# Optimization experiments

Hardware: AMD Instinct MI355X
Metric: run time of the kernel (lower is better)

The kernel has to match this reference:

```python
import jax, jax.numpy as jnp
import numpy as np

B, N, E, F_IN, F_OUT, HEADS, HDIM = 64, 1024, 16384, 300, 8, 4, 32
ALPHA = 0.5
BETA = float(np.log(0.1 / 2 + 1.0))  # GCN2Conv: theta=0.1, layer=2


def _norm(src, dst, ew, n):
    # GCN normalization with added self loops: D^-1/2 (A + I) D^-1/2, edge-list form
    idx = jnp.arange(n)
    r = jnp.concatenate([src, idx])
    c = jnp.concatenate([dst, idx])
    w = jnp.concatenate([ew, jnp.ones((n,), ew.dtype)])
    deg = jax.ops.segment_sum(w, c, num_segments=n)  # deg >= 1 (self loop weight 1)
    dinv = jax.lax.rsqrt(jnp.maximum(deg, 1e-12))
    return r, c, dinv[r] * w * dinv[c]


def _prop(h, r, c, w, n):
    # out[c] += w * h[r]  (source-to-target message passing)
    return jax.ops.segment_sum(w[:, None] * h[r], c, num_segments=n)


def _forward(edge_index, x, edge_weight, W1, b1, W2, b2, W3, b3, W4, b4, Wl, Wr, att, bg, Wg1, Wm, bm, Wg2, Wp1, bp1, Wp2, bp2, Wo, bo):
    def per_graph(xg, ei, ewg):
        src, dst = ei[0], ei[1]
        n = xg.shape[0]
        r, c, w = _norm(src, dst, ewg, n)                    # weighted gcn norm
        r1, c1, w1 = _norm(src, dst, jnp.ones_like(ewg), n)  # unweighted gcn norm
        h1 = jax.nn.relu(_prop(xg @ W1, r, c, w, n) + b1)    # [n,256]
        h2 = jax.nn.relu(_prop(h1 @ W2, r, c, w, n) + b2)    # [n,128]
        h = jax.nn.relu(_prop(h2 @ W3, r, c, w, n) + b3)     # [n,64]
        h = jax.nn.relu(_prop(h @ W4, r, c, w, n) + b4)      # [n,32]
        # GATv2Conv(32, 32, heads=4), self loops, concat heads, eval mode (no dropout)
        idx = jnp.arange(n)
        s2, d2 = jnp.concatenate([src, idx]), jnp.concatenate([dst, idx])
        xl = (h @ Wl).reshape(n, HEADS, HDIM)  # source transform
        xr = (h @ Wr).reshape(n, HEADS, HDIM)  # target transform
        e = jax.nn.leaky_relu(xl[s2] + xr[d2], 0.2)          # [E2,H,C]
        lg = jnp.einsum('ehc,hc->eh', e, att)                # [E2,H]
        mx = jax.ops.segment_max(lg, d2, num_segments=n)
        a = jnp.exp(lg - mx[d2])
        alpha = a / jax.ops.segment_sum(a, d2, num_segments=n)[d2]
        h = jax.ops.segment_sum(alpha[..., None] * xl[s2], d2, num_segments=n).reshape(n, HEADS * HDIM) + bg
        h = jax.nn.relu(h)                                   # [n,128]
        # GCN2Conv(128, alpha=0.5, theta=0.1, layer=2), x0 = h2, shared weights, no bias
        z = (1.0 - ALPHA) * _prop(h, r, c, w, n) + ALPHA * h2
        h = jax.nn.relu((1.0 - BETA) * z + BETA * (z @ Wg1))
        # GCNConv(128, 256) called WITHOUT edge weights
        h = jax.nn.relu(_prop(h @ Wm, r1, c1, w1, n) + bm)
        # GCN2Conv(256, 0.5, 0.1, 2), x0 = h1
        z = (1.0 - ALPHA) * _prop(h, r, c, w, n) + ALPHA * h1
        h = jax.nn.relu((1.0 - BETA) * z + BETA * (z @ Wg2))  # [n,256]
        # dense_diff_pool stage 1: GCNConv(256,5) soft assignments + to_dense_adj
        s = jax.nn.softmax(_prop(h @ Wp1, r, c, w, n) + bp1, axis=-1)  # [n,5]
        adj = jnp.zeros((n, n), h.dtype).at[src, dst].add(ewg)
        nodes = s.T @ h                                      # [5,256]
        adj2 = s.T @ adj @ s                                 # [5,5]
        # DenseGCNConv(256,1): set diag to 1, sym-normalize, propagate
        di = jnp.arange(5)
        adjl = adj2.at[di, di].set(1.0)
        dd = jax.lax.rsqrt(jnp.maximum(adjl.sum(-1), 1.0))
        sc = jax.nn.softmax((dd[:, None] * adjl * dd[None, :]) @ (nodes @ Wp2) + bp2, axis=-1)  # [5,1]
        # dense_diff_pool stage 2
        return (sc.T @ nodes)[0]                             # [256]

    pooled = jax.vmap(per_graph)(x, edge_index, edge_weight)  # [B,256]
    return pooled @ Wo + bo


def setup_inputs():
    key = jax.random.key(0)
    ks = jax.random.split(key, 32)
    lin = lambda k, fi, fo: jax.random.normal(k, (fi, fo), jnp.float32) / np.sqrt(fi)
    return {
        'x': jax.random.normal(ks[0], (B, N, F_IN), jnp.float32),
        'edge_index': jax.random.randint(ks[1], (B, 2, E), 0, N),
        'edge_weight': jax.random.uniform(ks[2], (B, E), jnp.float32),
        'W1': lin(ks[3], F_IN, 256), 'b1': jnp.zeros((256,), jnp.float32),
        'W2': lin(ks[4], 256, 128), 'b2': jnp.zeros((128,), jnp.float32),
        'W3': lin(ks[5], 128, 64), 'b3': jnp.zeros((64,), jnp.float32),
        'W4': lin(ks[6], 64, 32), 'b4': jnp.zeros((32,), jnp.float32),
        'Wl': lin(ks[7], 32, 128), 'Wr': lin(ks[8], 32, 128),
        'att': jax.random.normal(ks[9], (HEADS, HDIM), jnp.float32) / np.sqrt(HDIM),
        'bg': jnp.zeros((128,), jnp.float32),
        'Wg1': lin(ks[10], 128, 128),
        'Wm': lin(ks[11], 128, 256), 'bm': jnp.zeros((256,), jnp.float32),
        'Wg2': lin(ks[12], 256, 256),
        'Wp1': lin(ks[13], 256, 5), 'bp1': jnp.zeros((5,), jnp.float32),
        'Wp2': lin(ks[14], 256, 1), 'bp2': jnp.zeros((1,), jnp.float32),
        'Wo': lin(ks[15], 256, F_OUT), 'bo': jnp.zeros((F_OUT,), jnp.float32),
    }


def reference(x, edge_index, edge_weight, W1, b1, W2, b2, W3, b3, W4, b4, Wl, Wr, att, bg, Wg1, Wm, bm, Wg2, Wp1, bp1, Wp2, bp2, Wo, bo):
    return _forward(edge_index, x, edge_weight, W1, b1, W2, b2, W3, b3, W4, b4, Wl, Wr, att, bg, Wg1, Wm, bm, Wg2, Wp1, bp1, Wp2, bp2, Wo, bo)
```

## Files before the change

kernel.cpp:

```cpp
#include <hip/hip_runtime.h>
#include <cstdint>
#include <cstddef>

constexpr int NB = 64;
constexpr int NN = 1024;
constexpr int NE = 16384;
constexpr int NCH = 8;
constexpr int CHE = NE / NCH;
constexpr float C_BETA = 0.04879016417f;

typedef __attribute__((ext_vector_type(8))) short s8v;
typedef __attribute__((ext_vector_type(4))) float f4v;

__device__ inline float bf2f(ushort u){ union{uint u;float f;} v; v.u=((uint)u)<<16; return v.f; }
__device__ inline ushort f2bf(float f){ union{float f;uint u;} v; v.f=f; uint r=v.u+0x7fffu+((v.u>>16)&1u); return (ushort)(r>>16); }
__device__ inline void up8(uint4 x, float* o){
  o[0]=bf2f((ushort)x.x); o[1]=bf2f((ushort)(x.x>>16));
  o[2]=bf2f((ushort)x.y); o[3]=bf2f((ushort)(x.y>>16));
  o[4]=bf2f((ushort)x.z); o[5]=bf2f((ushort)(x.z>>16));
  o[6]=bf2f((ushort)x.w); o[7]=bf2f((ushort)(x.w>>16));
}
__device__ inline uint pk2(float a, float b){ return (uint)f2bf(a) | ((uint)f2bf(b)<<16); }
__device__ inline uint4 pk8(const float* f){
  uint4 v; v.x=pk2(f[0],f[1]); v.y=pk2(f[2],f[3]); v.z=pk2(f[4],f[5]); v.w=pk2(f[6],f[7]); return v;
}
__device__ inline int swz8(int bid, int bpg){
  int xcd = bid & 7, j = bid >> 3;
  return (xcd * (NB/8) + j / bpg) * bpg + (j % bpg);
}


__global__ __launch_bounds__(256) void hist_k(const int* __restrict__ ei,
    const float* __restrict__ ew, int* __restrict__ phist, float* __restrict__ pdegw) {
  int blk = blockIdx.x;
  int b = blk >> 3, ch = blk & 7;
  __shared__ int hc[NN];
  __shared__ float hw[NN];
  int t = threadIdx.x;
  for (int i = t; i < NN; i += 256) { hc[i] = 0; hw[i] = 0.f; }
  __syncthreads();
  const int* dstb = ei + (size_t)b * 2 * NE + NE + ch * CHE;
  const float* ewb = ew + (size_t)b * NE + ch * CHE;
  for (int e = t; e < CHE; e += 256) {
    int d = dstb[e];
    atomicAdd(&hc[d], 1);
    atomicAdd(&hw[d], ewb[e]);
  }
  __syncthreads();
  size_t o = ((size_t)b * NCH + ch) * NN;
  for (int i = t; i < NN; i += 256) {
    phist[o + i] = hc[i];
    pdegw[o + i] = hw[i];
  }
}


__global__ __launch_bounds__(1024) void scan2_k(int* __restrict__ phist,
    const float* __restrict__ pdegw, float* __restrict__ dinvw,
    float* __restrict__ dinvu, int* __restrict__ rowptr) {
  int b = blockIdx.x, t = threadIdx.x;
  size_t base = (size_t)b * NCH * NN;
  int h[NCH];
  int cnt = 0; float dw = 1.0f;
#pragma unroll
  for (int c = 0; c < NCH; ++c) {
    h[c] = phist[base + c * NN + t];
    cnt += h[c];
    dw += pdegw[base + c * NN + t];
  }
  dinvw[b * NN + t] = rsqrtf(dw);
  dinvu[b * NN + t] = rsqrtf(1.0f + (float)cnt);
  __shared__ int ss[NN];
  ss[t] = cnt;
  __syncthreads();
  for (int off = 1; off < NN; off <<= 1) {
    int xv = (t >= off) ? ss[t - off] : 0;
    __syncthreads();
    ss[t] += xv;
    __syncthreads();
  }
  rowptr[b * (NN + 1) + t + 1] = ss[t];
  if (t == 0) rowptr[b * (NN + 1)] = 0;
  int excl = ss[t] - cnt;
#pragma unroll
  for (int c = 0; c < NCH; ++c) {
    phist[base + c * NN + t] = excl;
    excl += h[c];
  }
}


__global__ __launch_bounds__(256) void scatter2_k(const int* __restrict__ ei,
    const float* __restrict__ ew, const int* __restrict__ coff,
    const float* __restrict__ dinvw, const float* __restrict__ dinvu,
    int4* __restrict__ pedge) {
  int blk = blockIdx.x;
  int b = blk >> 3, ch = blk & 7;
  __shared__ int sbase[NN];
  __shared__ int sfill[NN];
  __shared__ float sdw[NN];
  __shared__ float sdu[NN];
  int t = threadIdx.x;
  for (int i = t; i < NN; i += 256) {
    sbase[i] = coff[((size_t)b * NCH + ch) * NN + i];
    sfill[i] = 0;
    sdw[i] = dinvw[b * NN + i];
    sdu[i] = dinvu[b * NN + i];
  }
  __syncthreads();
  const int* srcb = ei + (size_t)b * 2 * NE + ch * CHE;
  const int* dstb = ei + (size_t)b * 2 * NE + NE + ch * CHE;
  const float* ewb = ew + (size_t)b * NE + ch * CHE;
  int4* peb = pedge + (size_t)b * NE;
  for (int e = t; e < CHE; e += 256) {
    int s = srcb[e], d = dstb[e];
    int pos = sbase[d] + atomicAdd(&sfill[d], 1);
    int4 pk;
    pk.x = s;
    pk.y = __float_as_int(sdw[s] * ewb[e] * sdw[d]);
    pk.z = __float_as_int(sdu[s] * sdu[d]);
    pk.w = 0;
    peb[pos] = pk;
  }
}


__global__ void xconv_k(const float* __restrict__ x, ushort* __restrict__ xbf) {
  int g = blockIdx.x * 256 + threadIdx.x;
  int row = g / 40, c = (g % 40) * 8;
  float f[8];
  const float* xr = x + (size_t)row * 300;
  if (c + 8 <= 300) {
    float4 a = *(const float4*)&xr[c];
    float4 bq = *(const float4*)&xr[c + 4];
    f[0]=a.x; f[1]=a.y; f[2]=a.z; f[3]=a.w;
    f[4]=bq.x; f[5]=bq.y; f[6]=bq.z; f[7]=bq.w;
  } else {
#pragma unroll
    for (int j = 0; j < 8; ++j) f[j] = (c + j < 300) ? xr[c + j] : 0.f;
  }
  *(uint4*)&xbf[(size_t)row * 320 + c] = pk8(f);
}

__device__ inline void wcv(const float* __restrict__ W, ushort* __restrict__ Wt,
                           int idx, int K, int N, int Kp) {
  int n = idx / Kp, k = idx % Kp;
  Wt[idx] = (k < K) ? f2bf(W[(size_t)k * N + n]) : (ushort)0;
}

__global__ void wconv_all_k(const float* W1, const float* W2, const float* W3,
                            const float* W4, const float* Wl, const float* Wr,
                            const float* Wg1, const float* Wm, const float* Wg2,
                            ushort* Wt1, ushort* Wt2, ushort* Wt3, ushort* Wt4,
                            ushort* WtLR, ushort* Wtg1, ushort* Wtm, ushort* Wtg2) {
  int bb = blockIdx.x, t = threadIdx.x;
  if      (bb < 320) wcv(W1, Wt1, bb * 256 + t, 300, 256, 320);
  else if (bb < 448) wcv(W2, Wt2, (bb - 320) * 256 + t, 256, 128, 256);
  else if (bb < 480) wcv(W3, Wt3, (bb - 448) * 256 + t, 128, 64, 128);
  else if (bb < 488) wcv(W4, Wt4, (bb - 480) * 256 + t, 64, 32, 64);
  else if (bb < 504) wcv(Wl, WtLR, (bb - 488) * 256 + t, 32, 128, 32);
  else if (bb < 520) wcv(Wr, WtLR + 128 * 32, (bb - 504) * 256 + t, 32, 128, 32);
  else if (bb < 584) wcv(Wg1, Wtg1, (bb - 520) * 256 + t, 128, 128, 128);
  else if (bb < 712) wcv(Wm, Wtm, (bb - 584) * 256 + t, 128, 256, 128);
  else               wcv(Wg2, Wtg2, (bb - 712) * 256 + t, 256, 256, 256);
}


template<int NI, int MODE>
__global__ __launch_bounds__(256) void mgemm_k(const ushort* __restrict__ A,
    const ushort* __restrict__ Bt, const ushort* __restrict__ Z,
    ushort* __restrict__ C, int M, int K, int N) {
  constexpr int BN = NI * 32;
  __shared__ ushort As[128][40];
  __shared__ ushort Bs[BN][40];
  int tid = threadIdx.x;
  int wave = tid >> 6, lane = tid & 63;
  int bm = blockIdx.y * 128, bn = blockIdx.x * BN;
  int wm = (wave >> 1) * 64, wn = (wave & 1) * (NI * 16);
  f4v acc[4][NI];
#pragma unroll
  for (int a = 0; a < 4; ++a)
#pragma unroll
    for (int b = 0; b < NI; ++b)
#pragma unroll
      for (int q = 0; q < 4; ++q) acc[a][b][q] = 0.f;
  int r = lane & 15, kg = (lane >> 4) * 8;
  for (int k0 = 0; k0 < K; k0 += 32) {
#pragma unroll
    for (int c = tid; c < 512; c += 256) {
      int row = c >> 2, kc = (c & 3) * 8;
      *(uint4*)&As[row][kc] = *(const uint4*)&A[(size_t)(bm + row) * K + k0 + kc];
    }
#pragma unroll
    for (int c = tid; c < BN * 4; c += 256) {
      int col = c >> 2, kc = (c & 3) * 8;
      *(uint4*)&Bs[col][kc] = *(const uint4*)&Bt[(size_t)(bn + col) * K + k0 + kc];
    }
    __syncthreads();
    s8v af[4], bf[NI];
#pragma unroll
    for (int mi = 0; mi < 4; ++mi) af[mi] = *(const s8v*)&As[wm + mi * 16 + r][kg];
#pragma unroll
    for (int ni = 0; ni < NI; ++ni) bf[ni] = *(const s8v*)&Bs[wn + ni * 16 + r][kg];
#pragma unroll
    for (int mi = 0; mi < 4; ++mi)
#pragma unroll
      for (int ni = 0; ni < NI; ++ni)
        acc[mi][ni] = __builtin_amdgcn_mfma_f32_16x16x32_bf16(af[mi], bf[ni], acc[mi][ni], 0, 0, 0);
    __syncthreads();
  }
  int col = lane & 15, rowg = (lane >> 4) * 4;
#pragma unroll
  for (int mi = 0; mi < 4; ++mi)
#pragma unroll
    for (int ni = 0; ni < NI; ++ni)
#pragma unroll
      for (int q = 0; q < 4; ++q) {
        int row = bm + wm + mi * 16 + rowg + q;
        int cc = bn + wn + ni * 16 + col;
        size_t idx = (size_t)row * N + cc;
        float v = acc[mi][ni][q];
        if (MODE == 2) v = fmaxf((1.f - C_BETA) * bf2f(Z[idx]) + C_BETA * v, 0.f);
        C[idx] = f2bf(v);
      }
}


template<int D, int MODE, int WSEL>
__global__ __launch_bounds__(256) void prop_k(const ushort* __restrict__ in,
    ushort* __restrict__ out, const int4* __restrict__ pedge,
    const float* __restrict__ dinv, const int* __restrict__ rowptr,
    const float* __restrict__ bias, const ushort* __restrict__ x0) {
  constexpr int TPN = D / 8, NPB = 256 / TPN, BPG = NN / NPB;
  int t = threadIdx.x;
  int bid = swz8(blockIdx.x, BPG);
  int tn = t / TPN, cl = t % TPN;
  int node = bid * NPB + tn;
  int b = node >> 10, i = node & 1023;
  float di = dinv[node];
  float f[8], acc[8];
  uint4 ov = *(const uint4*)&in[(size_t)node * D + cl * 8];
  up8(ov, f);
  float w0 = di * di;
#pragma unroll
  for (int j = 0; j < 8; ++j) acc[j] = w0 * f[j];
  int r0 = rowptr[b * (NN + 1) + i], r1 = rowptr[b * (NN + 1) + i + 1];
  const int4* pe = pedge + (size_t)b * NE;
  const ushort* inb = in + (size_t)b * NN * D;
  int p = r0;
  for (; p + 4 <= r1; p += 4) {
    int4 e0 = pe[p], e1 = pe[p + 1], e2 = pe[p + 2], e3 = pe[p + 3];
    float wa = __int_as_float(WSEL ? e0.z : e0.y);
    float wb2 = __int_as_float(WSEL ? e1.z : e1.y);
    float wc = __int_as_float(WSEL ? e2.z : e2.y);
    float wd = __int_as_float(WSEL ? e3.z : e3.y);
    uint4 rv0 = *(const uint4*)&inb[(size_t)e0.x * D + cl * 8];
    uint4 rv1 = *(const uint4*)&inb[(size_t)e1.x * D + cl * 8];
    uint4 rv2 = *(const uint4*)&inb[(size_t)e2.x * D + cl * 8];
    uint4 rv3 = *(const uint4*)&inb[(size_t)e3.x * D + cl * 8];
    up8(rv0, f);
#pragma unroll
    for (int j = 0; j < 8; ++j) acc[j] += wa * f[j];
    up8(rv1, f);
#pragma unroll
    for (int j = 0; j < 8; ++j) acc[j] += wb2 * f[j];
    up8(rv2, f);
#pragma unroll
    for (int j = 0; j < 8; ++j) acc[j] += wc * f[j];
    up8(rv3, f);
#pragma unroll
    for (int j = 0; j < 8; ++j) acc[j] += wd * f[j];
  }
  for (; p < r1; ++p) {
    int4 e = pe[p];
    float w = __int_as_float(WSEL ? e.z : e.y);
    uint4 rv = *(const uint4*)&inb[(size_t)e.x * D + cl * 8];
    up8(rv, f);
#pragma unroll
    for (int j = 0; j < 8; ++j) acc[j] += w * f[j];
  }
  size_t ob = (size_t)node * D + cl * 8;
  if (MODE == 0) {
#pragma unroll
    for (int j = 0; j < 8; ++j) acc[j] = fmaxf(acc[j] + bias[cl * 8 + j], 0.f);
  } else {
    uint4 xv = *(const uint4*)&x0[ob];
    up8(xv, f);
#pragma unroll
    for (int j = 0; j < 8; ++j) acc[j] = 0.5f * acc[j] + 0.5f * f[j];
  }
  *(uint4*)&out[ob] = pk8(acc);
}


__global__ __launch_bounds__(256) void gat_fused_k(const ushort* __restrict__ xlr,
    const int4* __restrict__ pedge, const int* __restrict__ rowptr,
    const float* __restrict__ att, const float* __restrict__ bg,
    ushort* __restrict__ out) {
  int bid = swz8(blockIdx.x, NN / 16);
  int t = threadIdx.x;
  int tn = t >> 4, cl = t & 15;
  int node = bid * 16 + tn;
  int b = node >> 10, i = node & 1023;
  int ch = cl * 8;
  int r0 = rowptr[b * (NN + 1) + i], r1 = rowptr[b * (NN + 1) + i + 1];
  const ushort* xb = xlr + (size_t)b * NN * 256;
  const int4* pe = pedge + (size_t)b * NE;
  float fr[8], at[8];
  {
    uint4 rv = *(const uint4*)&xb[(size_t)i * 256 + 128 + ch];
    up8(rv, fr);
#pragma unroll
    for (int j = 0; j < 8; ++j) at[j] = att[ch + j];
  }
  float m, den, acc[8];
  {
    float fs[8];
    uint4 sv = *(const uint4*)&xb[(size_t)i * 256 + ch];
    up8(sv, fs);
    float part = 0.f;
#pragma unroll
    for (int j = 0; j < 8; ++j) {
      float v = fs[j] + fr[j];
      v = v > 0.f ? v : 0.2f * v;
      part += v * at[j];
    }
    part += __shfl_xor(part, 1);
    part += __shfl_xor(part, 2);
    m = part; den = 1.f;
#pragma unroll
    for (int j = 0; j < 8; ++j) acc[j] = fs[j];
  }
  float fl0[8], fl1[8];
  int p = r0;
  for (; p + 2 <= r1; p += 2) {
    int s0 = pe[p].x, s1 = pe[p + 1].x;
    uint4 v0 = *(const uint4*)&xb[(size_t)s0 * 256 + ch];
    uint4 v1 = *(const uint4*)&xb[(size_t)s1 * 256 + ch];
    up8(v0, fl0); up8(v1, fl1);
    float p0 = 0.f, p1 = 0.f;
#pragma unroll
    for (int j = 0; j < 8; ++j) {
      float a0 = fl0[j] + fr[j]; a0 = a0 > 0.f ? a0 : 0.2f * a0;
      float a1 = fl1[j] + fr[j]; a1 = a1 > 0.f ? a1 : 0.2f * a1;
      p0 += a0 * at[j]; p1 += a1 * at[j];
    }
    p0 += __shfl_xor(p0, 1); p0 += __shfl_xor(p0, 2);
    p1 += __shfl_xor(p1, 1); p1 += __shfl_xor(p1, 2);
    {
      float mn = fmaxf(m, p0);
      float sc = __expf(m - mn), ex = __expf(p0 - mn);
      den = den * sc + ex;
#pragma unroll
      for (int j = 0; j < 8; ++j) acc[j] = acc[j] * sc + ex * fl0[j];
      m = mn;
    }
    {
      float mn = fmaxf(m, p1);
      float sc = __expf(m - mn), ex = __expf(p1 - mn);
      den = den * sc + ex;
#pragma unroll
      for (int j = 0; j < 8; ++j) acc[j] = acc[j] * sc + ex * fl1[j];
      m = mn;
    }
  }
  if (p < r1) {
    int s = pe[p].x;
    uint4 v0 = *(const uint4*)&xb[(size_t)s * 256 + ch];
    up8(v0, fl0);
    float p0 = 0.f;
#pragma unroll
    for (int j = 0; j < 8; ++j) {
      float a0 = fl0[j] + fr[j]; a0 = a0 > 0.f ? a0 : 0.2f * a0;
      p0 += a0 * at[j];
    }
    p0 += __shfl_xor(p0, 1); p0 += __shfl_xor(p0, 2);
    float mn = fmaxf(m, p0);
    float sc = __expf(m - mn), ex = __expf(p0 - mn);
    den = den * sc + ex;
#pragma unroll
    for (int j = 0; j < 8; ++j) acc[j] = acc[j] * sc + ex * fl0[j];
    m = mn;
  }
  float inv = 1.f / den;
#pragma unroll
  for (int j = 0; j < 8; ++j) acc[j] = fmaxf(acc[j] * inv + bg[ch + j], 0.f);
  *(uint4*)&out[(size_t)node * 128 + ch] = pk8(acc);
}


__global__ __launch_bounds__(256) void pool_part_k(const ushort* __restrict__ h7,
                                                   float* __restrict__ part) {
  int bid = blockIdx.x;
  int bgr = bid >> 3, seg = bid & 7;
  int t = threadIdx.x;
  int rg = t >> 5, cl = t & 31;
  const ushort* hb = h7 + (size_t)bgr * NN * 256;
  float a[8] = {};
  float f[8];
  for (int r = seg * 128 + rg; r < seg * 128 + 128; r += 8) {
    uint4 v = *(const uint4*)&hb[(size_t)r * 256 + cl * 8];
    up8(v, f);
#pragma unroll
    for (int j = 0; j < 8; ++j) a[j] += f[j];
  }
  __shared__ float red[8][256];
#pragma unroll
  for (int j = 0; j < 8; ++j) red[rg][cl * 8 + j] = a[j];
  __syncthreads();
  float s = 0.f;
#pragma unroll
  for (int g = 0; g < 8; ++g) s += red[g][t];
  part[(size_t)bid * 256 + t] = s;
}

__global__ __launch_bounds__(256) void pool_out_k(const float* __restrict__ part,
    const float* __restrict__ Wo, const float* __restrict__ bo, float* __restrict__ out) {
  int bgr = blockIdx.x, t = threadIdx.x;
  float s = 0.f;
#pragma unroll
  for (int g = 0; g < 8; ++g) s += part[(size_t)(bgr * 8 + g) * 256 + t];
  __shared__ float pv[256];
  pv[t] = s;
  __syncthreads();
  if (t < 8) {
    float o = bo[t];
    for (int c = 0; c < 256; ++c) o += pv[c] * Wo[c * 8 + t];
    out[bgr * 8 + t] = o;
  }
}

__global__ void zero_out_k(float* out, int n) {
  int g = blockIdx.x * 256 + threadIdx.x;
  if (g < n) out[g] = 0.f;
}


extern "C" void kernel_launch(void* const* d_in, const int* in_sizes, int n_in,
                              void* d_out, int out_size, void* d_ws, size_t ws_size,
                              hipStream_t stream) {
  const float* x   = (const float*)d_in[0];
  const int*   ei  = (const int*)d_in[1];
  const float* ew  = (const float*)d_in[2];
  const float* W1  = (const float*)d_in[3];
  const float* b1  = (const float*)d_in[4];
  const float* W2  = (const float*)d_in[5];
  const float* b2  = (const float*)d_in[6];
  const float* W3  = (const float*)d_in[7];
  const float* b3  = (const float*)d_in[8];
  const float* W4  = (const float*)d_in[9];
  const float* b4  = (const float*)d_in[10];
  const float* Wl  = (const float*)d_in[11];
  const float* Wr  = (const float*)d_in[12];
  const float* att = (const float*)d_in[13];
  const float* bg  = (const float*)d_in[14];
  const float* Wg1 = (const float*)d_in[15];
  const float* Wm  = (const float*)d_in[16];
  const float* bm  = (const float*)d_in[17];
  const float* Wg2 = (const float*)d_in[18];
  const float* Wo  = (const float*)d_in[23];
  const float* bo  = (const float*)d_in[24];
  float* out = (float*)d_out;

  const int M = NB * NN;

  char* wp = (char*)d_ws;
  size_t used = 0;
  auto alloc = [&](size_t bytes) -> void* {
    void* p = (void*)wp;
    size_t a = (bytes + 255) & ~(size_t)255;
    wp += a; used += a;
    return p;
  };
  float* dinvw = (float*)alloc((size_t)NB * NN * 4);
  float* dinvu = (float*)alloc((size_t)NB * NN * 4);
  int*   rowptr= (int*)alloc((size_t)NB * (NN + 1) * 4);
  int*   phist = (int*)alloc((size_t)NB * NCH * NN * 4);
  float* pdegw = (float*)alloc((size_t)NB * NCH * NN * 4);
  int4*  pedge = (int4*)alloc((size_t)NB * NE * 16);
  float* part  = (float*)alloc((size_t)NB * 8 * 256 * 4);
  ushort* xbf  = (ushort*)alloc((size_t)M * 320 * 2);
  ushort* Wt1  = (ushort*)alloc((size_t)256 * 320 * 2);
  ushort* Wt2  = (ushort*)alloc((size_t)128 * 256 * 2);
  ushort* Wt3  = (ushort*)alloc((size_t)64 * 128 * 2);
  ushort* Wt4  = (ushort*)alloc((size_t)32 * 64 * 2);
  ushort* WtLR = (ushort*)alloc((size_t)256 * 32 * 2);
  ushort* Wtg1 = (ushort*)alloc((size_t)128 * 128 * 2);
  ushort* Wtm  = (ushort*)alloc((size_t)256 * 128 * 2);
  ushort* Wtg2 = (ushort*)alloc((size_t)256 * 256 * 2);
  ushort* B1 = (ushort*)alloc((size_t)M * 256 * 2);
  ushort* B2 = (ushort*)alloc((size_t)M * 256 * 2);
  ushort* B3 = (ushort*)alloc((size_t)M * 256 * 2);
  ushort* B4 = (ushort*)alloc((size_t)M * 256 * 2);
  ushort* B2a = B2, *B2b = B2 + (size_t)M * 128;
  ushort* B3a = B3, *B3b = B3 + (size_t)M * 128;

  if (used > ws_size) {
    zero_out_k<<<(out_size + 255) / 256, 256, 0, stream>>>(out, out_size);
    return;
  }

  hist_k<<<NB * NCH, 256, 0, stream>>>(ei, ew, phist, pdegw);
  scan2_k<<<NB, 1024, 0, stream>>>(phist, pdegw, dinvw, dinvu, rowptr);
  scatter2_k<<<NB * NCH, 256, 0, stream>>>(ei, ew, phist, dinvw, dinvu, pedge);

  xconv_k<<<M * 40 / 256, 256, 0, stream>>>(x, xbf);
  wconv_all_k<<<968, 256, 0, stream>>>(W1, W2, W3, W4, Wl, Wr, Wg1, Wm, Wg2,
                                       Wt1, Wt2, Wt3, Wt4, WtLR, Wtg1, Wtm, Wtg2);

  mgemm_k<4,0><<<dim3(2, M / 128), 256, 0, stream>>>(xbf, Wt1, nullptr, B2, M, 320, 256);
  prop_k<256,0,0><<<M / 8, 256, 0, stream>>>(B2, B1, pedge, dinvw, rowptr, b1, nullptr);
  mgemm_k<4,0><<<dim3(1, M / 128), 256, 0, stream>>>(B1, Wt2, nullptr, B2a, M, 256, 128);
  prop_k<128,0,0><<<M / 16, 256, 0, stream>>>(B2a, B3a, pedge, dinvw, rowptr, b2, nullptr);
  mgemm_k<2,0><<<dim3(1, M / 128), 256, 0, stream>>>(B3a, Wt3, nullptr, B2a, M, 128, 64);
  prop_k<64,0,0><<<M / 32, 256, 0, stream>>>(B2a, B3b, pedge, dinvw, rowptr, b3, nullptr);
  mgemm_k<1,0><<<dim3(1, M / 128), 256, 0, stream>>>(B3b, Wt4, nullptr, B2a, M, 64, 32);
  prop_k<32,0,0><<<M / 64, 256, 0, stream>>>(B2a, B2b, pedge, dinvw, rowptr, b4, nullptr);

  mgemm_k<4,0><<<dim3(2, M / 128), 256, 0, stream>>>(B2b, WtLR, nullptr, B4, M, 32, 256);
  gat_fused_k<<<M / 16, 256, 0, stream>>>(B4, pedge, rowptr, att, bg, B2a);

  prop_k<128,1,0><<<M / 16, 256, 0, stream>>>(B2a, B2b, pedge, dinvw, rowptr, nullptr, B3a);
  mgemm_k<4,2><<<dim3(1, M / 128), 256, 0, stream>>>(B2b, Wtg1, B2b, B2a, M, 128, 128);

  mgemm_k<4,0><<<dim3(2, M / 128), 256, 0, stream>>>(B2a, Wtm, nullptr, B3, M, 128, 256);
  prop_k<256,0,1><<<M / 8, 256, 0, stream>>>(B3, B2, pedge, dinvu, rowptr, bm, nullptr);

  prop_k<256,1,0><<<M / 8, 256, 0, stream>>>(B2, B3, pedge, dinvw, rowptr, nullptr, B1);
  mgemm_k<4,2><<<dim3(2, M / 128), 256, 0, stream>>>(B3, Wtg2, B3, B2, M, 256, 256);

  pool_part_k<<<NB * 8, 256, 0, stream>>>(B2, part);
  pool_out_k<<<NB, 256, 0, stream>>>(part, Wo, bo, out);
}
```

Before: 492.0 us.

## Stage per-graph feature slices in LDS for propagation; lazy GAT softmax rescale

Rewrites the GCN propagation kernel so each block loads a graph's 32-column feature slice into shared memory (XOR-swizzled) and performs all neighbor gathers from LDS while iterating over all 1024 nodes in 16 passes. This replaces scattered global/L2 gathers with one coalesced load per slice. It reduces grid size substantially (as few as 64 blocks for D=32) and uses 64 KB LDS per block, limiting occupancy. The GAT online softmax now only rescales when a new logit exceeds the running max by more than 8, and leaky relu uses fmaxf.

Result: slower. 847.6 us (+72.3%).

```diff
diff --git a/kernel.cpp b/kernel.cpp
--- a/kernel.cpp
+++ b/kernel.cpp
@@ -54,7 +54,6 @@
   }
 }
 
-
 __global__ __launch_bounds__(1024) void scan2_k(int* __restrict__ phist,
     const float* __restrict__ pdegw, float* __restrict__ dinvw,
     float* __restrict__ dinvu, int* __restrict__ rowptr) {
@@ -88,7 +87,6 @@
     excl += h[c];
   }
 }
-
 
 __global__ __launch_bounds__(256) void scatter2_k(const int* __restrict__ ei,
     const float* __restrict__ ew, const int* __restrict__ coff,
@@ -227,71 +225,94 @@
 
 
 template<int D, int MODE, int WSEL>
-__global__ __launch_bounds__(256) void prop_k(const ushort* __restrict__ in,
+__global__ __launch_bounds__(256) void prop_lds_k(const ushort* __restrict__ in,
     ushort* __restrict__ out, const int4* __restrict__ pedge,
     const float* __restrict__ dinv, const int* __restrict__ rowptr,
     const float* __restrict__ bias, const ushort* __restrict__ x0) {
-  constexpr int TPN = D / 8, NPB = 256 / TPN, BPG = NN / NPB;
+  constexpr int NSL = D / 32;
+  __shared__ uint4 sf[4096];
+  int bid = swz8(blockIdx.x, NSL);
+  int b = bid / NSL, sl = bid % NSL;
+  int c0 = sl * 32;
   int t = threadIdx.x;
-  int bid = swz8(blockIdx.x, BPG);
-  int tn = t / TPN, cl = t % TPN;
-  int node = bid * NPB + tn;
-  int b = node >> 10, i = node & 1023;
-  float di = dinv[node];
-  float f[8], acc[8];
-  uint4 ov = *(const uint4*)&in[(size_t)node * D + cl * 8];
-  up8(ov, f);
-  float w0 = di * di;
-#pragma unroll
-  for (int j = 0; j < 8; ++j) acc[j] = w0 * f[j];
-  int r0 = rowptr[b * (NN + 1) + i], r1 = rowptr[b * (NN + 1) + i + 1];
+  const ushort* inb = in + (size_t)b * NN * D + c0;
+  for (int idx = t; idx < 4096; idx += 256) {
+    int i = idx >> 2, c = idx & 3;
+    sf[(i << 2) | (c ^ (i & 3))] = *(const uint4*)&inb[(size_t)i * D + c * 8];
+  }
+  __syncthreads();
+  int tn = t >> 2, cl = t & 3;
   const int4* pe = pedge + (size_t)b * NE;
-  const ushort* inb = in + (size_t)b * NN * D;
-  int p = r0;
-  for (; p + 4 <= r1; p += 4) {
-    int4 e0 = pe[p], e1 = pe[p + 1], e2 = pe[p + 2], e3 = pe[p + 3];
-    float wa = __int_as_float(WSEL ? e0.z : e0.y);
-    float wb2 = __int_as_float(WSEL ? e1.z : e1.y);
-    float wc = __int_as_float(WSEL ? e2.z : e2.y);
-    float wd = __int_as_float(WSEL ? e3.z : e3.y);
-    uint4 rv0 = *(const uint4*)&inb[(size_t)e0.x * D + cl * 8];
-    uint4 rv1 = *(const uint4*)&inb[(size_t)e1.x * D + cl * 8];
-    uint4 rv2 = *(const uint4*)&inb[(size_t)e2.x * D + cl * 8];
-    uint4 rv3 = *(const uint4*)&inb[(size_t)e3.x * D + cl * 8];
-    up8(rv0, f);
-#pragma unroll
-    for (int j = 0; j < 8; ++j) acc[j] += wa * f[j];
-    up8(rv1, f);
-#pragma unroll
-    for (int j = 0; j < 8; ++j) acc[j] += wb2 * f[j];
-    up8(rv2, f);
-#pragma unroll
-    for (int j = 0; j < 8; ++j) acc[j] += wc * f[j];
-    up8(rv3, f);
-#pragma unroll
-    for (int j = 0; j < 8; ++j) acc[j] += wd * f[j];
-  }
-  for (; p < r1; ++p) {
-    int4 e = pe[p];
-    float w = __int_as_float(WSEL ? e.z : e.y);
-    uint4 rv = *(const uint4*)&inb[(size_t)e.x * D + cl * 8];
-    up8(rv, f);
-#pragma unroll
-    for (int j = 0; j < 8; ++j) acc[j] += w * f[j];
-  }
-  size_t ob = (size_t)node * D + cl * 8;
+  const int* rp = rowptr + b * (NN + 1);
+  float bi[8];
   if (MODE == 0) {
 #pragma unroll
-    for (int j = 0; j < 8; ++j) acc[j] = fmaxf(acc[j] + bias[cl * 8 + j], 0.f);
-  } else {
-    uint4 xv = *(const uint4*)&x0[ob];
-    up8(xv, f);
-#pragma unroll
-    for (int j = 0; j < 8; ++j) acc[j] = 0.5f * acc[j] + 0.5f * f[j];
-  }
-  *(uint4*)&out[ob] = pk8(acc);
-}
-
+    for (int j = 0; j < 8; ++j) bi[j] = bias[c0 + cl * 8 + j];
+  }
+#pragma unroll 1
+  for (int pass = 0; pass < 16; ++pass) {
+    int i = pass * 64 + tn;
+    float di = dinv[b * NN + i];
+    float f[8], acc[8];
+    uint4 sv = sf[(i << 2) | (cl ^ (i & 3))];
+    up8(sv, f);
+    float w0 = di * di;
+#pragma unroll
+    for (int j = 0; j < 8; ++j) acc[j] = w0 * f[j];
+    int r0 = rp[i], r1 = rp[i + 1];
+    int p = r0;
+    for (; p + 2 <= r1; p += 2) {
+      int4 e0 = pe[p], e1 = pe[p + 1];
+      float wa = __int_as_float(WSEL ? e0.z : e0.y);
+      float wb = __int_as_float(WSEL ? e1.z : e1.y);
+      uint4 v0 = sf[(e0.x << 2) | (cl ^ (e0.x & 3))];
+      uint4 v1 = sf[(e1.x << 2) | (cl ^ (e1.x & 3))];
+      up8(v0, f);
+#pragma unroll
+      for (int j = 0; j < 8; ++j) acc[j] += wa * f[j];
+      up8(v1, f);
+#pragma unroll
+      for (int j = 0; j < 8; ++j) acc[j] += wb * f[j];
+    }
+    if (p < r1) {
+      int4 e = pe[p];
+      float w = __int_as_float(WSEL ? e.z : e.y);
+      uint4 v = sf[(e.x << 2) | (cl ^ (e.x & 3))];
+      up8(v, f);
+#pragma unroll
+      for (int j = 0; j < 8; ++j) acc[j] += w * f[j];
+    }
+    size_t ob = ((size_t)b * NN + i) * D + c0 + cl * 8;
+    if (MODE == 0) {
+#pragma unroll
+      for (int j = 0; j < 8; ++j) acc[j] = fmaxf(acc[j] + bi[j], 0.f);
+    } else {
+      uint4 xv = *(const uint4*)&x0[ob];
+      up8(xv, f);
+#pragma unroll
+      for (int j = 0; j < 8; ++j) acc[j] = 0.5f * acc[j] + 0.5f * f[j];
+    }
+    *(uint4*)&out[ob] = pk8(acc);
+  }
+}
+
+
+#define GAT_UPD(P, FL)                                            \
+  if (P > m + 8.f) {                           \
+    float sc = __expf(m - P);                                     \
+    den *= sc;                                                    \
+    _Pragma("unroll")                                             \
+    for (int j = 0; j < 8; ++j) acc[j] *= sc;                     \
+    m = P;                                                        \
+    den += 1.f;                                                   \
+    _Pragma("unroll")                                             \
+    for (int j = 0; j < 8; ++j) acc[j] += FL[j];                  \
+  } else {                                                        \
+    float ex = __expf(P - m);                                     \
+    den += ex;                                                    \
+    _Pragma("unroll")                                             \
+    for (int j = 0; j < 8; ++j) acc[j] += ex * FL[j];             \
+  }
 
 __global__ __launch_bounds__(256) void gat_fused_k(const ushort* __restrict__ xlr,
     const int4* __restrict__ pedge, const int* __restrict__ rowptr,
@@ -322,8 +343,7 @@
 #pragma unroll
     for (int j = 0; j < 8; ++j) {
       float v = fs[j] + fr[j];
-      v = v > 0.f ? v : 0.2f * v;
-      part += v * at[j];
+      part += fmaxf(v, 0.2f * v) * at[j];
     }
     part += __shfl_xor(part, 1);
     part += __shfl_xor(part, 2);
@@ -341,28 +361,15 @@
     float p0 = 0.f, p1 = 0.f;
 #pragma unroll
     for (int j = 0; j < 8; ++j) {
-      float a0 = fl0[j] + fr[j]; a0 = a0 > 0.f ? a0 : 0.2f * a0;
-      float a1 = fl1[j] + fr[j]; a1 = a1 > 0.f ? a1 : 0.2f * a1;
-      p0 += a0 * at[j]; p1 += a1 * at[j];
+      float a0 = fl0[j] + fr[j];
+      float a1 = fl1[j] + fr[j];
+      p0 += fmaxf(a0, 0.2f * a0) * at[j];
+      p1 += fmaxf(a1, 0.2f * a1) * at[j];
     }
     p0 += __shfl_xor(p0, 1); p0 += __shfl_xor(p0, 2);
     p1 += __shfl_xor(p1, 1); p1 += __shfl_xor(p1, 2);
-    {
-      float mn = fmaxf(m, p0);
-      float sc = __expf(m - mn), ex = __expf(p0 - mn);
-      den = den * sc + ex;
-#pragma unroll
-      for (int j = 0; j < 8; ++j) acc[j] = acc[j] * sc + ex * fl0[j];
-      m = mn;
-    }
-    {
-      float mn = fmaxf(m, p1);
-      float sc = __expf(m - mn), ex = __expf(p1 - mn);
-      den = den * sc + ex;
-#pragma unroll
-      for (int j = 0; j < 8; ++j) acc[j] = acc[j] * sc + ex * fl1[j];
-      m = mn;
-    }
+    GAT_UPD(p0, fl0)
+    GAT_UPD(p1, fl1)
   }
   if (p < r1) {
     int s = pe[p].x;
@@ -371,16 +378,11 @@
     float p0 = 0.f;
 #pragma unroll
     for (int j = 0; j < 8; ++j) {
-      float a0 = fl0[j] + fr[j]; a0 = a0 > 0.f ? a0 : 0.2f * a0;
-      p0 += a0 * at[j];
+      float a0 = fl0[j] + fr[j];
+      p0 += fmaxf(a0, 0.2f * a0) * at[j];
     }
     p0 += __shfl_xor(p0, 1); p0 += __shfl_xor(p0, 2);
-    float mn = fmaxf(m, p0);
-    float sc = __expf(m - mn), ex = __expf(p0 - mn);
-    den = den * sc + ex;
-#pragma unroll
-    for (int j = 0; j < 8; ++j) acc[j] = acc[j] * sc + ex * fl0[j];
-    m = mn;
+    GAT_UPD(p0, fl0)
   }
   float inv = 1.f / den;
 #pragma unroll
@@ -509,24 +511,24 @@
                                        Wt1, Wt2, Wt3, Wt4, WtLR, Wtg1, Wtm, Wtg2);
 
   mgemm_k<4,0><<<dim3(2, M / 128), 256, 0, stream>>>(xbf, Wt1, nullptr, B2, M, 320, 256);
-  prop_k<256,0,0><<<M / 8, 256, 0, stream>>>(B2, B1, pedge, dinvw, rowptr, b1, nullptr);
+  prop_lds_k<256,0,0><<<NB * 8, 256, 0, stream>>>(B2, B1, pedge, dinvw, rowptr, b1, nullptr);
   mgemm_k<4,0><<<dim3(1, M / 128), 256, 0, stream>>>(B1, Wt2, nullptr, B2a, M, 256, 128);
-  prop_k<128,0,0><<<M / 16, 256, 0, stream>>>(B2a, B3a, pedge, dinvw, rowptr, b2, nullptr);
+  prop_lds_k<128,0,0><<<NB * 4, 256, 0, stream>>>(B2a, B3a, pedge, dinvw, rowptr, b2, nullptr);
   mgemm_k<2,0><<<dim3(1, M / 128), 256, 0, stream>>>(B3a, Wt3, nullptr, B2a, M, 128, 64);
-  prop_k<64,0,0><<<M / 32, 256, 0, stream>>>(B2a, B3b, pedge, dinvw, rowptr, b3, nullptr);
+  prop_lds_k<64,0,0><<<NB * 2, 256, 0, stream>>>(B2a, B3b, pedge, dinvw, rowptr, b3, nullptr);
   mgemm_k<1,0><<<dim3(1, M / 128), 256, 0, stream>>>(B3b, Wt4, nullptr, B2a, M, 64, 32);
-  prop_k<32,0,0><<<M / 64, 256, 0, stream>>>(B2a, B2b, pedge, dinvw, rowptr, b4, nullptr);
+  prop_lds_k<32,0,0><<<NB, 256, 0, stream>>>(B2a, B2b, pedge, dinvw, rowptr, b4, nullptr);
 
   mgemm_k<4,0><<<dim3(2, M / 128), 256, 0, stream>>>(B2b, WtLR, nullptr, B4, M, 32, 256);
   gat_fused_k<<<M / 16, 256, 0, stream>>>(B4, pedge, rowptr, att, bg, B2a);
 
-  prop_k<128,1,0><<<M / 16, 256, 0, stream>>>(B2a, B2b, pedge, dinvw, rowptr, nullptr, B3a);
+  prop_lds_k<128,1,0><<<NB * 4, 256, 0, stream>>>(B2a, B2b, pedge, dinvw, rowptr, nullptr, B3a);
   mgemm_k<4,2><<<dim3(1, M / 128), 256, 0, stream>>>(B2b, Wtg1, B2b, B2a, M, 128, 128);
 
   mgemm_k<4,0><<<dim3(2, M / 128), 256, 0, stream>>>(B2a, Wtm, nullptr, B3, M, 128, 256);
-  prop_k<256,0,1><<<M / 8, 256, 0, stream>>>(B3, B2, pedge, dinvu, rowptr, bm, nullptr);
-
-  prop_k<256,1,0><<<M / 8, 256, 0, stream>>>(B2, B3, pedge, dinvw, rowptr, nullptr, B1);
+  prop_lds_k<256,0,1><<<NB * 8, 256, 0, stream>>>(B3, B2, pedge, dinvu, rowptr, bm, nullptr);
+
+  prop_lds_k<256,1,0><<<NB * 8, 256, 0, stream>>>(B2, B3, pedge, dinvw, rowptr, nullptr, B1);
   mgemm_k<4,2><<<dim3(2, M / 128), 256, 0, stream>>>(B3, Wtg2, B3, B2, M, 256, 256);
 
   pool_part_k<<<NB * 8, 256, 0, stream>>>(B2, part);
```
